# Performance work log

Hardware: AMD Instinct MI355X
Metric: run time of the kernel (lower is better)

The kernel has to match this reference:

```python
import jax, jax.numpy as jnp
import numpy as np

H = 50  # LSTM hidden size (fixed in source)


def setup_inputs() -> dict:
    key = jax.random.key(0)
    ks = jax.random.split(key, 8)
    B, T, P = 1024, 1024, 16
    s = 1.0 / np.sqrt(H)  # torch LSTM/Linear default init scale
    return {
        "x": jax.random.normal(ks[0], (B, T, 1), dtype=jnp.float32),
        "params": jax.random.normal(ks[1], (B, T, P), dtype=jnp.float32),
        "W_ih": jax.random.uniform(ks[2], (4 * H, 1), dtype=jnp.float32, minval=-s, maxval=s),
        "W_hh": jax.random.uniform(ks[3], (4 * H, H), dtype=jnp.float32, minval=-s, maxval=s),
        "b_ih": jax.random.uniform(ks[4], (4 * H,), dtype=jnp.float32, minval=-s, maxval=s),
        "b_hh": jax.random.uniform(ks[5], (4 * H,), dtype=jnp.float32, minval=-s, maxval=s),
        "W_lin": jax.random.uniform(ks[6], (1, H + P), dtype=jnp.float32, minval=-s, maxval=s),
        "b_lin": jax.random.uniform(ks[7], (1,), dtype=jnp.float32, minval=-s, maxval=s),
    }


def _lstm(x, W_ih, W_hh, b_ih, b_hh):
    # x: [B, T, 1] -> hidden sequence [B, T, H]. PyTorch gate order: i, f, g, o.
    B = x.shape[0]
    # Precompute input contribution for all timesteps: [B, T, 4H]
    xg = jnp.einsum('bti,gi->btg', x, W_ih) + b_ih + b_hh
    xg_t = jnp.swapaxes(xg, 0, 1)  # [T, B, 4H]

    def step(carry, g_in):
        h, c = carry
        gates = g_in + h @ W_hh.T  # [B, 4H]
        i, f, g, o = jnp.split(gates, 4, axis=-1)
        c = jax.nn.sigmoid(f) * c + jax.nn.sigmoid(i) * jnp.tanh(g)
        h = jax.nn.sigmoid(o) * jnp.tanh(c)
        return (h, c), h

    h0 = jnp.zeros((B, H), dtype=x.dtype)
    c0 = jnp.zeros((B, H), dtype=x.dtype)
    (_, _), hs = jax.lax.scan(step, (h0, c0), xg_t)
    return jnp.swapaxes(hs, 0, 1)  # [B, T, H]


def reference(x, params, W_ih, W_hh, b_ih, b_hh, W_lin, b_lin):
    hs = _lstm(x, W_ih, W_hh, b_ih, b_hh)            # [B, T, H]
    combined = jnp.concatenate((hs, params), axis=2)  # [B, T, H+P]
    return jnp.einsum('btf,of->bto', combined, W_lin) + b_lin  # [B, T, 1]
```

## Files before the change

### kernel.cpp

```cpp
#include <hip/hip_runtime.h>
#include <stdint.h>

namespace {

constexpr int Bn = 1024;
constexpr int Tn = 1024;
constexpr int Hn = 50;
constexpr int Pn = 16;
constexpr int KP = 25;

typedef _Float16 h2 __attribute__((ext_vector_type(2)));

__device__ __forceinline__ float fast_rcp(float x) { return __builtin_amdgcn_rcpf(x); }
__device__ __forceinline__ float fast_sigmoid(float x) {
    return fast_rcp(1.0f + __expf(-x));
}
__device__ __forceinline__ float fast_tanh(float x) {
    return 1.0f - 2.0f * fast_rcp(__expf(2.0f * x) + 1.0f);
}
__device__ __forceinline__ float fdot2(h2 a, h2 b, float c) {
    return __builtin_amdgcn_fdot2(a, b, c, false);
}

__global__ __attribute__((amdgpu_flat_work_group_size(64, 64), amdgpu_waves_per_eu(1, 1)))
void lstm_core_h(const float* __restrict__ x, const float* __restrict__ W_ih,
                 const float* __restrict__ W_hh, const float* __restrict__ b_ih,
                 const float* __restrict__ b_hh, uint32_t* __restrict__ hbuf)
{
    const int b    = blockIdx.x;
    const int lane = threadIdx.x;
    const int jj   = (lane < Hn) ? lane : Hn - 1;

    h2 w0[KP], w1[KP], w2[KP], w3[KP];
    const float* r0 = W_hh + (size_t)(0 * Hn + jj) * Hn;
    const float* r1 = W_hh + (size_t)(1 * Hn + jj) * Hn;
    const float* r2 = W_hh + (size_t)(2 * Hn + jj) * Hn;
    const float* r3 = W_hh + (size_t)(3 * Hn + jj) * Hn;
    #pragma unroll
    for (int k = 0; k < KP; ++k) {
        w0[k] = h2{(_Float16)r0[2 * k], (_Float16)r0[2 * k + 1]};
        w1[k] = h2{(_Float16)r1[2 * k], (_Float16)r1[2 * k + 1]};
        w2[k] = h2{(_Float16)r2[2 * k], (_Float16)r2[2 * k + 1]};
        w3[k] = h2{(_Float16)r3[2 * k], (_Float16)r3[2 * k + 1]};
    }
    #pragma unroll
    for (int k = 0; k < KP; ++k) {
        asm volatile("" : "+v"(w0[k]), "+v"(w1[k]), "+v"(w2[k]), "+v"(w3[k]));
    }

    const float wih0 = W_ih[0 * Hn + jj];
    const float wih1 = W_ih[1 * Hn + jj];
    const float wih2 = W_ih[2 * Hn + jj];
    const float wih3 = W_ih[3 * Hn + jj];
    const float bb0 = b_ih[0 * Hn + jj] + b_hh[0 * Hn + jj];
    const float bb1 = b_ih[1 * Hn + jj] + b_hh[1 * Hn + jj];
    const float bb2 = b_ih[2 * Hn + jj] + b_hh[2 * Hn + jj];
    const float bb3 = b_ih[3 * Hn + jj] + b_hh[3 * Hn + jj];

    const float4* xb4 = (const float4*)(x + (size_t)b * Tn);

    uint32_t* hb = hbuf + ((size_t)b * KP + (size_t)(lane >> 1)) * Tn;
    const bool writer = (lane < Hn) && ((lane & 1) == 0);

    float h = 0.0f, c = 0.0f;
    int sp[KP];
    #pragma unroll
    for (int k = 0; k < KP; ++k) sp[k] = 0;

    float4 xA = xb4[0];

    for (int tt = 0; tt < Tn / 4; ++tt) {
        float4 xB = make_float4(0.f, 0.f, 0.f, 0.f);
        if (tt + 1 < Tn / 4) xB = xb4[tt + 1];

        const float xs[4] = {xA.x, xA.y, xA.z, xA.w};

        #pragma unroll
        for (int u = 0; u < 4; ++u) {
            float a0 = fmaf(xs[u], wih0, bb0);
            float a1 = fmaf(xs[u], wih1, bb1);
            float a2 = fmaf(xs[u], wih2, bb2);
            float a3 = fmaf(xs[u], wih3, bb3);
            #pragma unroll
            for (int k = 0; k < KP; ++k) {
                const h2 hp = __builtin_bit_cast(h2, sp[k]);
                a0 = fdot2(hp, w0[k], a0);
                a1 = fdot2(hp, w1[k], a1);
                a2 = fdot2(hp, w2[k], a2);
                a3 = fdot2(hp, w3[k], a3);
            }

            const float ig = fast_sigmoid(a0);
            const float fg = fast_sigmoid(a1);
            const float gg = fast_tanh(a2);
            const float og = fast_sigmoid(a3);
            c = fmaf(fg, c, ig * gg);
            h = og * fast_tanh(c);

            const int hi = __builtin_bit_cast(int, h);
            const int hj = __builtin_amdgcn_update_dpp(0, hi, 0xB1, 0xF, 0xF, true);
            const int packed = __builtin_bit_cast(int,
                __builtin_amdgcn_cvt_pkrtz(h, __builtin_bit_cast(float, hj)));

            if (writer) hb[tt * 4 + u] = (uint32_t)packed;

            #pragma unroll
            for (int k = 0; k < KP; ++k)
                sp[k] = __builtin_amdgcn_readlane(packed, 2 * k);
        }
        xA = xB;
    }
}

__global__ __launch_bounds__(256)
void post_proj(const uint32_t* __restrict__ hbuf, const float* __restrict__ params,
               const float* __restrict__ W_lin, const float* __restrict__ b_lin,
               float* __restrict__ out)
{
    const int i = blockIdx.x * 256 + threadIdx.x;
    const int b = i >> 10;
    const int t = i & (Tn - 1);

    float s = b_lin[0];
    const uint32_t* hp = hbuf + (size_t)b * KP * Tn + t;
    #pragma unroll
    for (int k = 0; k < KP; ++k) {
        const h2 wlk = h2{(_Float16)W_lin[2 * k], (_Float16)W_lin[2 * k + 1]};
        s = fdot2(__builtin_bit_cast(h2, hp[(size_t)k * Tn]), wlk, s);
    }

    const float4* p4 = (const float4*)(params + (size_t)i * Pn);
    const float4 a = p4[0], bq = p4[1], cq = p4[2], dq = p4[3];
    const float* wp = W_lin + Hn;
    s += a.x  * wp[ 0] + a.y  * wp[ 1] + a.z  * wp[ 2] + a.w  * wp[ 3];
    s += bq.x * wp[ 4] + bq.y * wp[ 5] + bq.z * wp[ 6] + bq.w * wp[ 7];
    s += cq.x * wp[ 8] + cq.y * wp[ 9] + cq.z * wp[10] + cq.w * wp[11];
    s += dq.x * wp[12] + dq.y * wp[13] + dq.z * wp[14] + dq.w * wp[15];
    out[i] = s;
}

__global__ __launch_bounds__(256)
void params_proj(const float* __restrict__ params, const float* __restrict__ W_lin,
                 float* __restrict__ pp)
{
    const int i = blockIdx.x * 256 + threadIdx.x;
    const float4* p4 = (const float4*)(params + (size_t)i * Pn);
    const float4 a = p4[0], b = p4[1], c = p4[2], d = p4[3];
    const float* wl = W_lin + Hn;
    float s;
    s  = a.x * wl[ 0] + a.y * wl[ 1] + a.z * wl[ 2] + a.w * wl[ 3];
    s += b.x * wl[ 4] + b.y * wl[ 5] + b.z * wl[ 6] + b.w * wl[ 7];
    s += c.x * wl[ 8] + c.y * wl[ 9] + c.z * wl[10] + c.w * wl[11];
    s += d.x * wl[12] + d.y * wl[13] + d.z * wl[14] + d.w * wl[15];
    pp[i] = s;
}

__global__ __attribute__((amdgpu_flat_work_group_size(64, 64), amdgpu_waves_per_eu(1, 1)))
void lstm_core_fused(const float* __restrict__ x, const float* __restrict__ W_ih,
                     const float* __restrict__ W_hh, const float* __restrict__ b_ih,
                     const float* __restrict__ b_hh, const float* __restrict__ W_lin,
                     const float* __restrict__ b_lin, const float* __restrict__ pp,
                     float* __restrict__ out)
{
    const int b    = blockIdx.x;
    const int lane = threadIdx.x;
    const int jj   = (lane < Hn) ? lane : Hn - 1;

    h2 w0[KP], w1[KP], w2[KP], w3[KP], wl[KP];
    const float* r0 = W_hh + (size_t)(0 * Hn + jj) * Hn;
    const float* r1 = W_hh + (size_t)(1 * Hn + jj) * Hn;
    const float* r2 = W_hh + (size_t)(2 * Hn + jj) * Hn;
    const float* r3 = W_hh + (size_t)(3 * Hn + jj) * Hn;
    #pragma unroll
    for (int k = 0; k < KP; ++k) {
        w0[k] = h2{(_Float16)r0[2 * k], (_Float16)r0[2 * k + 1]};
        w1[k] = h2{(_Float16)r1[2 * k], (_Float16)r1[2 * k + 1]};
        w2[k] = h2{(_Float16)r2[2 * k], (_Float16)r2[2 * k + 1]};
        w3[k] = h2{(_Float16)r3[2 * k], (_Float16)r3[2 * k + 1]};
        wl[k] = h2{(_Float16)W_lin[2 * k], (_Float16)W_lin[2 * k + 1]};
    }
    #pragma unroll
    for (int k = 0; k < KP; ++k) {
        asm volatile("" : "+v"(w0[k]), "+v"(w1[k]), "+v"(w2[k]), "+v"(w3[k]), "+v"(wl[k]));
    }

    const float wih0 = W_ih[0 * Hn + jj];
    const float wih1 = W_ih[1 * Hn + jj];
    const float wih2 = W_ih[2 * Hn + jj];
    const float wih3 = W_ih[3 * Hn + jj];
    const float bb0 = b_ih[0 * Hn + jj] + b_hh[0 * Hn + jj];
    const float bb1 = b_ih[1 * Hn + jj] + b_hh[1 * Hn + jj];
    const float bb2 = b_ih[2 * Hn + jj] + b_hh[2 * Hn + jj];
    const float bb3 = b_ih[3 * Hn + jj] + b_hh[3 * Hn + jj];
    const float blin = b_lin[0];

    const float4* xb4 = (const float4*)(x + (size_t)b * Tn);
    const float4* pp4 = (const float4*)(pp + (size_t)b * Tn);
    float4* ob4 = (float4*)(out + (size_t)b * Tn);

    float h = 0.0f, c = 0.0f;
    int sp[KP];
    #pragma unroll
    for (int k = 0; k < KP; ++k) sp[k] = 0;

    float4 xA = xb4[0], pA = pp4[0];

    for (int tt = 0; tt < Tn / 4; ++tt) {
        float4 xB = make_float4(0.f, 0.f, 0.f, 0.f), pB = xB;
        if (tt + 1 < Tn / 4) { xB = xb4[tt + 1]; pB = pp4[tt + 1]; }

        const float xs[4] = {xA.x, xA.y, xA.z, xA.w};
        const float ps[4] = {pA.x, pA.y, pA.z, pA.w};
        float o4[4];

        #pragma unroll
        for (int u = 0; u < 4; ++u) {
            float a0 = fmaf(xs[u], wih0, bb0);
            float a1 = fmaf(xs[u], wih1, bb1);
            float a2 = fmaf(xs[u], wih2, bb2);
            float a3 = fmaf(xs[u], wih3, bb3);
            #pragma unroll
            for (int k = 0; k < KP; ++k) {
                const h2 hp = __builtin_bit_cast(h2, sp[k]);
                a0 = fdot2(hp, w0[k], a0);
                a1 = fdot2(hp, w1[k], a1);
                a2 = fdot2(hp, w2[k], a2);
                a3 = fdot2(hp, w3[k], a3);
            }

            const float ig = fast_sigmoid(a0);
            const float fg = fast_sigmoid(a1);
            const float gg = fast_tanh(a2);
            const float og = fast_sigmoid(a3);
            c = fmaf(fg, c, ig * gg);
            h = og * fast_tanh(c);

            const int hi = __builtin_bit_cast(int, h);
            const int hj = __builtin_amdgcn_update_dpp(0, hi, 0xB1, 0xF, 0xF, true);
            const int packed = __builtin_bit_cast(int,
                __builtin_amdgcn_cvt_pkrtz(h, __builtin_bit_cast(float, hj)));

            #pragma unroll
            for (int k = 0; k < KP; ++k)
                sp[k] = __builtin_amdgcn_readlane(packed, 2 * k);

            float prj = ps[u] + blin;
            #pragma unroll
            for (int k = 0; k < KP; ++k)
                prj = fdot2(__builtin_bit_cast(h2, sp[k]), wl[k], prj);
            o4[u] = prj;
        }

        if (lane == 0) ob4[tt] = make_float4(o4[0], o4[1], o4[2], o4[3]);
        xA = xB; pA = pB;
    }
}

}

extern "C" void kernel_launch(void* const* d_in, const int* in_sizes, int n_in,
                              void* d_out, int out_size, void* d_ws, size_t ws_size,
                              hipStream_t stream) {
    const float* x      = (const float*)d_in[0];
    const float* params = (const float*)d_in[1];
    const float* W_ih   = (const float*)d_in[2];
    const float* W_hh   = (const float*)d_in[3];
    const float* b_ih   = (const float*)d_in[4];
    const float* b_hh   = (const float*)d_in[5];
    const float* W_lin  = (const float*)d_in[6];
    const float* b_lin  = (const float*)d_in[7];
    float* out = (float*)d_out;

    const size_t hbuf_bytes = (size_t)Bn * KP * Tn * sizeof(uint32_t);

    if (ws_size >= hbuf_bytes) {
        uint32_t* hbuf = (uint32_t*)d_ws;
        lstm_core_h<<<dim3(Bn), dim3(64), 0, stream>>>(
            x, W_ih, W_hh, b_ih, b_hh, hbuf);
        post_proj<<<dim3(Bn * Tn / 256), dim3(256), 0, stream>>>(
            hbuf, params, W_lin, b_lin, out);
    } else {
        float* pp = (float*)d_ws;
        params_proj<<<dim3(Bn * Tn / 256), dim3(256), 0, stream>>>(params, W_lin, pp);
        lstm_core_fused<<<dim3(Bn), dim3(64), 0, stream>>>(
            x, W_ih, W_hh, b_ih, b_hh, W_lin, b_lin, pp, out);
    }
}
```

Before: 488.3 us.

## Split LSTM recurrence K-dimension across two waves with packed FP16 FMA

The recurrent matvec is split over two wavefronts per batch row, each holding half of the W_hh columns and computing partial gate sums. The partials are exchanged through double-buffered shared memory with a barrier every timestep. Accumulation changes from fp32 fdot2 to packed fp16 FMA, with the two halves reduced into fp32 at the end. The aim is to halve the serial dependent FMA chain per step, at the cost of a block barrier per step and reduced accumulation precision.

After: 665.1 us. 36.2% more time.

```diff
diff --git a/kernel.cpp b/kernel.cpp
--- a/kernel.cpp
+++ b/kernel.cpp
@@ -21,94 +21,156 @@
 __device__ __forceinline__ float fdot2(h2 a, h2 b, float c) {
     return __builtin_amdgcn_fdot2(a, b, c, false);
 }
-
-__global__ __attribute__((amdgpu_flat_work_group_size(64, 64), amdgpu_waves_per_eu(1, 1)))
-void lstm_core_h(const float* __restrict__ x, const float* __restrict__ W_ih,
-                 const float* __restrict__ W_hh, const float* __restrict__ b_ih,
-                 const float* __restrict__ b_hh, uint32_t* __restrict__ hbuf)
-{
+__device__ __forceinline__ h2 pkfma(h2 a, h2 b, h2 c) {
+    return __builtin_elementwise_fma(a, b, c);
+}
+
+template<int K0, int NK, bool HASX>
+__device__ __forceinline__ void run_tloop(
+    h2 (&w0)[NK], h2 (&w1)[NK], h2 (&w2)[NK], h2 (&w3)[NK],
+    float wih0, float wih1, float wih2, float wih3,
+    float bb0, float bb1, float bb2, float bb3,
+    const float4* __restrict__ xb4, uint32_t* __restrict__ hb, bool writer,
+    float4 (&part)[2][2][64], int wid, int lane)
+{
+    const h2 one2  = h2{(_Float16)1.0f, (_Float16)1.0f};
+    const h2 zero2 = h2{(_Float16)0.0f, (_Float16)0.0f};
+
+    float h = 0.0f, c = 0.0f;
+    int sp[NK];
+    #pragma unroll
+    for (int k = 0; k < NK; ++k) sp[k] = 0;
+
+    float4 xA = make_float4(0.f, 0.f, 0.f, 0.f);
+    if constexpr (HASX) xA = xb4[0];
+
+    for (int tt = 0; tt < Tn / 4; ++tt) {
+        float4 xB = make_float4(0.f, 0.f, 0.f, 0.f);
+        if constexpr (HASX) {
+            if (tt + 1 < Tn / 4) xB = xb4[tt + 1];
+        }
+        const float xs[4] = {xA.x, xA.y, xA.z, xA.w};
+
+        #pragma unroll
+        for (int u = 0; u < 4; ++u) {
+            h2 a0 = zero2, a1 = zero2, a2 = zero2, a3 = zero2;
+            #pragma unroll
+            for (int k = 0; k < NK; ++k) {
+                const h2 hp = __builtin_bit_cast(h2, sp[k]);
+                a0 = pkfma(hp, w0[k], a0);
+                a1 = pkfma(hp, w1[k], a1);
+                a2 = pkfma(hp, w2[k], a2);
+                a3 = pkfma(hp, w3[k], a3);
+            }
+            float s0, s1, s2, s3;
+            if constexpr (HASX) {
+                s0 = fdot2(a0, one2, fmaf(xs[u], wih0, bb0));
+                s1 = fdot2(a1, one2, fmaf(xs[u], wih1, bb1));
+                s2 = fdot2(a2, one2, fmaf(xs[u], wih2, bb2));
+                s3 = fdot2(a3, one2, fmaf(xs[u], wih3, bb3));
+            } else {
+                s0 = fdot2(a0, one2, 0.0f);
+                s1 = fdot2(a1, one2, 0.0f);
+                s2 = fdot2(a2, one2, 0.0f);
+                s3 = fdot2(a3, one2, 0.0f);
+            }
+
+            part[u & 1][wid][lane] = make_float4(s0, s1, s2, s3);
+            __syncthreads();
+            const float4 p = part[u & 1][wid ^ 1][lane];
+            s0 += p.x; s1 += p.y; s2 += p.z; s3 += p.w;
+
+            const float ig = fast_sigmoid(s0);
+            const float fg = fast_sigmoid(s1);
+            const float gg = fast_tanh(s2);
+            const float og = fast_sigmoid(s3);
+            c = fmaf(fg, c, ig * gg);
+            h = og * fast_tanh(c);
+
+            const int hi = __builtin_bit_cast(int, h);
+            const int hj = __builtin_amdgcn_update_dpp(0, hi, 0xB1, 0xF, 0xF, true);
+            const int packed = __builtin_bit_cast(int,
+                __builtin_amdgcn_cvt_pkrtz(h, __builtin_bit_cast(float, hj)));
+
+            if (writer) hb[tt * 4 + u] = (uint32_t)packed;
+
+            #pragma unroll
+            for (int k = 0; k < NK; ++k)
+                sp[k] = __builtin_amdgcn_readlane(packed, 2 * (K0 + k));
+        }
+        xA = xB;
+    }
+}
+
+__global__ __attribute__((amdgpu_flat_work_group_size(128, 128), amdgpu_waves_per_eu(2, 2)))
+void lstm_core_h2(const float* __restrict__ x, const float* __restrict__ W_ih,
+                  const float* __restrict__ W_hh, const float* __restrict__ b_ih,
+                  const float* __restrict__ b_hh, uint32_t* __restrict__ hbuf)
+{
+    __shared__ float4 part[2][2][64];
+
+    const int tid  = threadIdx.x;
+    const int lane = tid & 63;
+    const int wid  = __builtin_amdgcn_readfirstlane(tid >> 6);
     const int b    = blockIdx.x;
-    const int lane = threadIdx.x;
     const int jj   = (lane < Hn) ? lane : Hn - 1;
 
-    h2 w0[KP], w1[KP], w2[KP], w3[KP];
+    const float4* xb4 = (const float4*)(x + (size_t)b * Tn);
+    uint32_t* hb = hbuf + ((size_t)b * KP + (size_t)(lane >> 1)) * Tn;
+
     const float* r0 = W_hh + (size_t)(0 * Hn + jj) * Hn;
     const float* r1 = W_hh + (size_t)(1 * Hn + jj) * Hn;
     const float* r2 = W_hh + (size_t)(2 * Hn + jj) * Hn;
     const float* r3 = W_hh + (size_t)(3 * Hn + jj) * Hn;
-    #pragma unroll
-    for (int k = 0; k < KP; ++k) {
-        w0[k] = h2{(_Float16)r0[2 * k], (_Float16)r0[2 * k + 1]};
-        w1[k] = h2{(_Float16)r1[2 * k], (_Float16)r1[2 * k + 1]};
-        w2[k] = h2{(_Float16)r2[2 * k], (_Float16)r2[2 * k + 1]};
-        w3[k] = h2{(_Float16)r3[2 * k], (_Float16)r3[2 * k + 1]};
-    }
-    #pragma unroll
-    for (int k = 0; k < KP; ++k) {
-        asm volatile("" : "+v"(w0[k]), "+v"(w1[k]), "+v"(w2[k]), "+v"(w3[k]));
-    }
-
-    const float wih0 = W_ih[0 * Hn + jj];
-    const float wih1 = W_ih[1 * Hn + jj];
-    const float wih2 = W_ih[2 * Hn + jj];
-    const float wih3 = W_ih[3 * Hn + jj];
-    const float bb0 = b_ih[0 * Hn + jj] + b_hh[0 * Hn + jj];
-    const float bb1 = b_ih[1 * Hn + jj] + b_hh[1 * Hn + jj];
-    const float bb2 = b_ih[2 * Hn + jj] + b_hh[2 * Hn + jj];
-    const float bb3 = b_ih[3 * Hn + jj] + b_hh[3 * Hn + jj];
-
-    const float4* xb4 = (const float4*)(x + (size_t)b * Tn);
-
-    uint32_t* hb = hbuf + ((size_t)b * KP + (size_t)(lane >> 1)) * Tn;
-    const bool writer = (lane < Hn) && ((lane & 1) == 0);
-
-    float h = 0.0f, c = 0.0f;
-    int sp[KP];
-    #pragma unroll
-    for (int k = 0; k < KP; ++k) sp[k] = 0;
-
-    float4 xA = xb4[0];
-
-    for (int tt = 0; tt < Tn / 4; ++tt) {
-        float4 xB = make_float4(0.f, 0.f, 0.f, 0.f);
-        if (tt + 1 < Tn / 4) xB = xb4[tt + 1];
-
-        const float xs[4] = {xA.x, xA.y, xA.z, xA.w};
-
-        #pragma unroll
-        for (int u = 0; u < 4; ++u) {
-            float a0 = fmaf(xs[u], wih0, bb0);
-            float a1 = fmaf(xs[u], wih1, bb1);
-            float a2 = fmaf(xs[u], wih2, bb2);
-            float a3 = fmaf(xs[u], wih3, bb3);
-            #pragma unroll
-            for (int k = 0; k < KP; ++k) {
-                const h2 hp = __builtin_bit_cast(h2, sp[k]);
-                a0 = fdot2(hp, w0[k], a0);
-                a1 = fdot2(hp, w1[k], a1);
-                a2 = fdot2(hp, w2[k], a2);
-                a3 = fdot2(hp, w3[k], a3);
-            }
-
-            const float ig = fast_sigmoid(a0);
-            const float fg = fast_sigmoid(a1);
-            const float gg = fast_tanh(a2);
-            const float og = fast_sigmoid(a3);
-            c = fmaf(fg, c, ig * gg);
-            h = og * fast_tanh(c);
-
-            const int hi = __builtin_bit_cast(int, h);
-            const int hj = __builtin_amdgcn_update_dpp(0, hi, 0xB1, 0xF, 0xF, true);
-            const int packed = __builtin_bit_cast(int,
-                __builtin_amdgcn_cvt_pkrtz(h, __builtin_bit_cast(float, hj)));
-
-            if (writer) hb[tt * 4 + u] = (uint32_t)packed;
-
-            #pragma unroll
-            for (int k = 0; k < KP; ++k)
-                sp[k] = __builtin_amdgcn_readlane(packed, 2 * k);
-        }
-        xA = xB;
+
+    if (wid == 0) {
+        constexpr int K0 = 0, NK = 13;
+        h2 w0[NK], w1[NK], w2[NK], w3[NK];
+        #pragma unroll
+        for (int k = 0; k < NK; ++k) {
+            const int g = 2 * (K0 + k);
+            w0[k] = h2{(_Float16)r0[g], (_Float16)r0[g + 1]};
+            w1[k] = h2{(_Float16)r1[g], (_Float16)r1[g + 1]};
+            w2[k] = h2{(_Float16)r2[g], (_Float16)r2[g + 1]};
+            w3[k] = h2{(_Float16)r3[g], (_Float16)r3[g + 1]};
+        }
+        #pragma unroll
+        for (int k = 0; k < NK; ++k)
+            asm volatile("" : "+v"(w0[k]), "+v"(w1[k]), "+v"(w2[k]), "+v"(w3[k]));
+
+        const bool writer = ((lane & 1) == 0) && ((lane >> 1) < K0 + NK);
+        run_tloop<K0, NK, false>(w0, w1, w2, w3,
+                                 0.f, 0.f, 0.f, 0.f, 0.f, 0.f, 0.f, 0.f,
+                                 xb4, hb, writer, part, wid, lane);
+    } else {
+        constexpr int K0 = 13, NK = 12;
+        h2 w0[NK], w1[NK], w2[NK], w3[NK];
+        #pragma unroll
+        for (int k = 0; k < NK; ++k) {
+            const int g = 2 * (K0 + k);
+            w0[k] = h2{(_Float16)r0[g], (_Float16)r0[g + 1]};
+            w1[k] = h2{(_Float16)r1[g], (_Float16)r1[g + 1]};
+            w2[k] = h2{(_Float16)r2[g], (_Float16)r2[g + 1]};
+            w3[k] = h2{(_Float16)r3[g], (_Float16)r3[g + 1]};
+        }
+        #pragma unroll
+        for (int k = 0; k < NK; ++k)
+            asm volatile("" : "+v"(w0[k]), "+v"(w1[k]), "+v"(w2[k]), "+v"(w3[k]));
+
+        const float wih0 = W_ih[0 * Hn + jj];
+        const float wih1 = W_ih[1 * Hn + jj];
+        const float wih2 = W_ih[2 * Hn + jj];
+        const float wih3 = W_ih[3 * Hn + jj];
+        const float bb0 = b_ih[0 * Hn + jj] + b_hh[0 * Hn + jj];
+        const float bb1 = b_ih[1 * Hn + jj] + b_hh[1 * Hn + jj];
+        const float bb2 = b_ih[2 * Hn + jj] + b_hh[2 * Hn + jj];
+        const float bb3 = b_ih[3 * Hn + jj] + b_hh[3 * Hn + jj];
+
+        const bool writer = ((lane & 1) == 0) && ((lane >> 1) >= K0) &&
+                            ((lane >> 1) < K0 + NK);
+        run_tloop<K0, NK, true>(w0, w1, w2, w3,
+                                wih0, wih1, wih2, wih3, bb0, bb1, bb2, bb3,
+                                xb4, hb, writer, part, wid, lane);
     }
 }
 
@@ -275,7 +337,7 @@
 
     if (ws_size >= hbuf_bytes) {
         uint32_t* hbuf = (uint32_t*)d_ws;
-        lstm_core_h<<<dim3(Bn), dim3(64), 0, stream>>>(
+        lstm_core_h2<<<dim3(Bn), dim3(128), 0, stream>>>(
             x, W_ih, W_hh, b_ih, b_hh, hbuf);
         post_proj<<<dim3(Bn * Tn / 256), dim3(256), 0, stream>>>(
             hbuf, params, W_lin, b_lin, out);
```
